# Kernel optimization log

Measured on AMD Instinct MI355X. Metric: run time of the kernel, lower is better.

## Reference

```python
import jax, jax.numpy as jnp
import numpy as np

N, M, D = 131072, 128, 128

def setup_inputs() -> dict:
    key = jax.random.key(0)
    k1, k2, k3 = jax.random.split(key, 3)
    X = jax.random.normal(k1, (N, D), dtype=jnp.float32)
    r = jax.random.uniform(k2, (N, M), dtype=jnp.float32)
    mus = jax.random.normal(k3, (M, D), dtype=jnp.float32)
    return {"X": X, "r": r, "mus": mus}

def reference(X, r, mus):
    # Squared pairwise L2 distances without materializing [N, M, D]:
    x2 = jnp.sum(X * X, axis=1)            # [N]
    mu2 = jnp.sum(mus * mus, axis=1)       # [M]
    cross = X @ mus.T                      # [N, M]
    dist2 = jnp.maximum(x2[:, None] + mu2[None, :] - 2.0 * cross, 0.0)
    loss = jnp.sum(r * dist2) / X.shape[0]
    return loss
```

## Files before the change

### kernel.cpp

```cpp
#include <hip/hip_runtime.h>
#include <hip/hip_bf16.h>


typedef __attribute__((ext_vector_type(8)))  short  short8;
typedef __attribute__((ext_vector_type(16))) float  float16v;

#if defined(__has_builtin)
#if __has_builtin(__builtin_amdgcn_cvt_pk_bf16_f32)
#define HAVE_PK_BF16 1
#endif
#endif

__device__ __forceinline__ unsigned int pk_bf16(float x, float y) {
#ifdef HAVE_PK_BF16
    typedef __attribute__((ext_vector_type(2))) __bf16 bf16x2;
    bf16x2 p = __builtin_amdgcn_cvt_pk_bf16_f32(x, y);
    return __builtin_bit_cast(unsigned int, p);
#else
    unsigned int ux = __float_as_uint(x);
    unsigned int uy = __float_as_uint(y);
    ux += 0x7fffu + ((ux >> 16) & 1u);
    uy += 0x7fffu + ((uy >> 16) & 1u);
    return (ux >> 16) | (uy & 0xffff0000u);
#endif
}

__global__ void zero_out_kernel(float* out) { out[0] = 0.0f; }

__global__ __launch_bounds__(256, 4)
void isoloss_kernel(const float* __restrict__ X,
                    const float* __restrict__ r,
                    const float* __restrict__ mus,
                    float* __restrict__ out)
{
    const int tid  = threadIdx.x;
    const int wave = tid >> 6;
    const int lane = tid & 63;
    const int col  = lane & 31;
    const int half = lane >> 5;

    __shared__ float wsum[4];

    short8 bfrag[8];
    float mu2p = 0.0f;
    {
        const float* mrow = mus + (size_t)(wave * 32 + col) * 128 + half * 8;
        #pragma unroll
        for (int ks = 0; ks < 8; ++ks) {
            const float4 a = *(const float4*)(mrow + ks * 16);
            const float4 b = *(const float4*)(mrow + ks * 16 + 4);
            mu2p += a.x*a.x + a.y*a.y + a.z*a.z + a.w*a.w
                  + b.x*b.x + b.y*b.y + b.z*b.z + b.w*b.w;
            union { short8 s8; uint4 u4; } u;
            u.u4.x = pk_bf16(a.x, a.y);
            u.u4.y = pk_bf16(a.z, a.w);
            u.u4.z = pk_bf16(b.x, b.y);
            u.u4.w = pk_bf16(b.z, b.w);
            bfrag[ks] = u.s8;
        }
    }
    const float mu2 = mu2p + __shfl_xor(mu2p, 32);

    float s = 0.0f;

    for (int g = blockIdx.x; g < 4096; g += gridDim.x) {
        const int rowbase = g * 32;
        const float* xp = X + (size_t)(rowbase + col) * 128 + half * 8;
        const float* rp = r + (size_t)rowbase * 128 + wave * 32 + col;

        float rv[16];
        #pragma unroll
        for (int reg = 0; reg < 16; ++reg) {
            const int rl = (reg & 3) + 8 * (reg >> 2) + 4 * half;
            rv[reg] = rp[(size_t)rl * 128];
        }

        float16v acc = {};
        float p = 0.0f;
        #pragma unroll
        for (int ks = 0; ks < 8; ++ks) {
            const float4 a = *(const float4*)(xp + ks * 16);
            const float4 b = *(const float4*)(xp + ks * 16 + 4);
            p += a.x*a.x + a.y*a.y + a.z*a.z + a.w*a.w
               + b.x*b.x + b.y*b.y + b.z*b.z + b.w*b.w;
            union { short8 s8; uint4 u4; } u;
            u.u4.x = pk_bf16(a.x, a.y);
            u.u4.y = pk_bf16(a.z, a.w);
            u.u4.z = pk_bf16(b.x, b.y);
            u.u4.w = pk_bf16(b.z, b.w);
            acc = __builtin_amdgcn_mfma_f32_32x32x16_bf16(u.s8, bfrag[ks], acc, 0, 0, 0);
        }
        const float x2v = p + __shfl_xor(p, 32);

        #pragma unroll
        for (int reg = 0; reg < 16; ++reg) {
            const int rl = (reg & 3) + 8 * (reg >> 2) + 4 * half;
            const float x2r = __shfl(x2v, rl);
            float d = fmaxf(x2r + mu2 - 2.0f * acc[reg], 0.0f);
            s += rv[reg] * d;
        }
    }

    #pragma unroll
    for (int off = 32; off > 0; off >>= 1) s += __shfl_down(s, off);
    if (lane == 0) wsum[wave] = s;
    __syncthreads();
    if (tid == 0) {
        const float t = wsum[0] + wsum[1] + wsum[2] + wsum[3];
        atomicAdd(out, t * (1.0f / 131072.0f));
    }
}

extern "C" void kernel_launch(void* const* d_in, const int* in_sizes, int n_in,
                              void* d_out, int out_size, void* d_ws, size_t ws_size,
                              hipStream_t stream) {
    const float* X   = (const float*)d_in[0];
    const float* r   = (const float*)d_in[1];
    const float* mus = (const float*)d_in[2];
    float* out = (float*)d_out;

    zero_out_kernel<<<1, 1, 0, stream>>>(out);
    isoloss_kernel<<<1024, 256, 0, stream>>>(X, r, mus, out);
}
```

Measured before the change: 171.8 us.

## Stage X tile in LDS as bf16 once per block and spread atomics

Each block now loads its 128-row X tile once with coalesced loads, computes row norms and bf16 conversions once, and stores them in LDS. All four waves then share them instead of each reloading and converting the same rows. The final sum goes through 64 workspace slots and a separate reduce kernel to reduce atomic contention. LDS use and register pressure increase, occupancy bounds drop, and there is an extra kernel launch.

```diff
diff --git a/kernel.cpp b/kernel.cpp
--- a/kernel.cpp
+++ b/kernel.cpp
@@ -4,6 +4,8 @@
 
 typedef __attribute__((ext_vector_type(8)))  short  short8;
 typedef __attribute__((ext_vector_type(16))) float  float16v;
+
+#define LDSP 136
 
 #if defined(__has_builtin)
 #if __has_builtin(__builtin_amdgcn_cvt_pk_bf16_f32)
@@ -25,21 +27,55 @@
 #endif
 }
 
-__global__ void zero_out_kernel(float* out) { out[0] = 0.0f; }
+__global__ void zero_ws_kernel(float* ws) { ws[threadIdx.x] = 0.0f; }
 
-__global__ __launch_bounds__(256, 4)
+__global__ void final_reduce_kernel(const float* ws, float* out) {
+    const int lane = threadIdx.x;
+    float t = ws[lane];
+    #pragma unroll
+    for (int off = 32; off > 0; off >>= 1) t += __shfl_down(t, off);
+    if (lane == 0) out[0] = t * (1.0f / 131072.0f);
+}
+
+__global__ __launch_bounds__(256, 3)
 void isoloss_kernel(const float* __restrict__ X,
                     const float* __restrict__ r,
                     const float* __restrict__ mus,
-                    float* __restrict__ out)
+                    float* __restrict__ ws)
 {
     const int tid  = threadIdx.x;
+    const int blk  = blockIdx.x;
     const int wave = tid >> 6;
     const int lane = tid & 63;
     const int col  = lane & 31;
     const int half = lane >> 5;
 
+    __shared__ unsigned short ldsA[128 * LDSP];
+    __shared__ float x2s[128];
     __shared__ float wsum[4];
+
+    const float* xbase = X + (size_t)blk * 128 * 128;
+    float4 xv[16];
+    #pragma unroll
+    for (int it = 0; it < 16; ++it)
+        xv[it] = *(const float4*)(xbase + (size_t)(it * 256 + tid) * 4);
+
+    #pragma unroll
+    for (int it = 0; it < 16; ++it) {
+        const float4 v = xv[it];
+        float p = v.x*v.x + v.y*v.y + v.z*v.z + v.w*v.w;
+        p += __shfl_xor(p, 16);
+        p += __shfl_xor(p, 8);
+        p += __shfl_xor(p, 4);
+        p += __shfl_xor(p, 2);
+        p += __shfl_xor(p, 1);
+        const int row = it * 8 + (tid >> 5);
+        if ((tid & 31) == 0) x2s[row] = p;
+        uint2 h;
+        h.x = pk_bf16(v.x, v.y);
+        h.y = pk_bf16(v.z, v.w);
+        *(uint2*)&ldsA[row * LDSP + (tid & 31) * 4] = h;
+    }
 
     short8 bfrag[8];
     float mu2p = 0.0f;
@@ -61,13 +97,12 @@
     }
     const float mu2 = mu2p + __shfl_xor(mu2p, 32);
 
+    __syncthreads();
+
     float s = 0.0f;
-
-    for (int g = blockIdx.x; g < 4096; g += gridDim.x) {
-        const int rowbase = g * 32;
-        const float* xp = X + (size_t)(rowbase + col) * 128 + half * 8;
-        const float* rp = r + (size_t)rowbase * 128 + wave * 32 + col;
-
+    #pragma unroll
+    for (int mt = 0; mt < 4; ++mt) {
+        const float* rp = r + (size_t)(blk * 128 + mt * 32) * 128 + wave * 32 + col;
         float rv[16];
         #pragma unroll
         for (int reg = 0; reg < 16; ++reg) {
@@ -76,27 +111,20 @@
         }
 
         float16v acc = {};
-        float p = 0.0f;
         #pragma unroll
         for (int ks = 0; ks < 8; ++ks) {
-            const float4 a = *(const float4*)(xp + ks * 16);
-            const float4 b = *(const float4*)(xp + ks * 16 + 4);
-            p += a.x*a.x + a.y*a.y + a.z*a.z + a.w*a.w
-               + b.x*b.x + b.y*b.y + b.z*b.z + b.w*b.w;
-            union { short8 s8; uint4 u4; } u;
-            u.u4.x = pk_bf16(a.x, a.y);
-            u.u4.y = pk_bf16(a.z, a.w);
-            u.u4.z = pk_bf16(b.x, b.y);
-            u.u4.w = pk_bf16(b.z, b.w);
-            acc = __builtin_amdgcn_mfma_f32_32x32x16_bf16(u.s8, bfrag[ks], acc, 0, 0, 0);
+            const short8 af = *(const short8*)&ldsA[(mt * 32 + col) * LDSP + ks * 16 + half * 8];
+            acc = __builtin_amdgcn_mfma_f32_32x32x16_bf16(af, bfrag[ks], acc, 0, 0, 0);
         }
-        const float x2v = p + __shfl_xor(p, 32);
+
+        float4 xq[4];
+        #pragma unroll
+        for (int q = 0; q < 4; ++q)
+            xq[q] = *(const float4*)&x2s[mt * 32 + q * 8 + half * 4];
 
         #pragma unroll
         for (int reg = 0; reg < 16; ++reg) {
-            const int rl = (reg & 3) + 8 * (reg >> 2) + 4 * half;
-            const float x2r = __shfl(x2v, rl);
-            float d = fmaxf(x2r + mu2 - 2.0f * acc[reg], 0.0f);
+            const float d = fmaxf(xq[reg >> 2][reg & 3] + mu2 - 2.0f * acc[reg], 0.0f);
             s += rv[reg] * d;
         }
     }
@@ -105,10 +133,8 @@
     for (int off = 32; off > 0; off >>= 1) s += __shfl_down(s, off);
     if (lane == 0) wsum[wave] = s;
     __syncthreads();
-    if (tid == 0) {
-        const float t = wsum[0] + wsum[1] + wsum[2] + wsum[3];
-        atomicAdd(out, t * (1.0f / 131072.0f));
-    }
+    if (tid == 0)
+        atomicAdd(&ws[blk & 63], wsum[0] + wsum[1] + wsum[2] + wsum[3]);
 }
 
 extern "C" void kernel_launch(void* const* d_in, const int* in_sizes, int n_in,
@@ -118,7 +144,9 @@
     const float* r   = (const float*)d_in[1];
     const float* mus = (const float*)d_in[2];
     float* out = (float*)d_out;
+    float* ws  = (float*)d_ws;
 
-    zero_out_kernel<<<1, 1, 0, stream>>>(out);
-    isoloss_kernel<<<1024, 256, 0, stream>>>(X, r, mus, out);
+    zero_ws_kernel<<<1, 64, 0, stream>>>(ws);
+    isoloss_kernel<<<1024, 256, 0, stream>>>(X, r, mus, ws);
+    final_reduce_kernel<<<1, 64, 0, stream>>>(ws, out);
 }
```

Measured after the change: 151.0 us. -12.1%, faster.

## Swap MFMA operands for vectorized r loads, prefetch X, spread atomics

Applied to the files above, without the earlier changes.

Swaps the MFMA A/B operands so each lane's accumulator holds a row of contiguous centroid columns, which lets r be read with float4 loads instead of 16 scalar strided loads. X is now loaded in two halves, with the second half issued as software prefetch inside the k-loop. mu2 values are pre-shuffled once outside the loop, which removes the per-element shuffles of x2. The single-address atomic is replaced by 64 workspace slots plus a final reduction kernel, at the cost of an extra launch. Launch bounds are lowered to 3 blocks per CU, giving more registers per thread.

```diff
diff --git a/kernel.cpp b/kernel.cpp
--- a/kernel.cpp
+++ b/kernel.cpp
@@ -25,13 +25,21 @@
 #endif
 }
 
-__global__ void zero_out_kernel(float* out) { out[0] = 0.0f; }
+__global__ void zero_ws_kernel(float* ws) { ws[threadIdx.x] = 0.0f; }
 
-__global__ __launch_bounds__(256, 4)
+__global__ void final_reduce_kernel(const float* ws, float* out) {
+    const int lane = threadIdx.x;
+    float t = ws[lane];
+    #pragma unroll
+    for (int off = 32; off > 0; off >>= 1) t += __shfl_down(t, off);
+    if (lane == 0) out[0] = t * (1.0f / 131072.0f);
+}
+
+__global__ __launch_bounds__(256, 3)
 void isoloss_kernel(const float* __restrict__ X,
                     const float* __restrict__ r,
                     const float* __restrict__ mus,
-                    float* __restrict__ out)
+                    float* __restrict__ ws)
 {
     const int tid  = threadIdx.x;
     const int wave = tid >> 6;
@@ -60,27 +68,43 @@
         }
     }
     const float mu2 = mu2p + __shfl_xor(mu2p, 32);
+    float4 mu2q[4];
+    #pragma unroll
+    for (int q = 0; q < 4; ++q) {
+        mu2q[q].x = __shfl(mu2, q * 8 + half * 4 + 0);
+        mu2q[q].y = __shfl(mu2, q * 8 + half * 4 + 1);
+        mu2q[q].z = __shfl(mu2, q * 8 + half * 4 + 2);
+        mu2q[q].w = __shfl(mu2, q * 8 + half * 4 + 3);
+    }
 
     float s = 0.0f;
 
     for (int g = blockIdx.x; g < 4096; g += gridDim.x) {
         const int rowbase = g * 32;
         const float* xp = X + (size_t)(rowbase + col) * 128 + half * 8;
-        const float* rp = r + (size_t)rowbase * 128 + wave * 32 + col;
+        const float* rp = r + (size_t)(rowbase + col) * 128 + wave * 32 + half * 4;
 
-        float rv[16];
+        float4 xa[4], xb[4];
         #pragma unroll
-        for (int reg = 0; reg < 16; ++reg) {
-            const int rl = (reg & 3) + 8 * (reg >> 2) + 4 * half;
-            rv[reg] = rp[(size_t)rl * 128];
+        for (int j = 0; j < 4; ++j) {
+            xa[j] = *(const float4*)(xp + j * 16);
+            xb[j] = *(const float4*)(xp + j * 16 + 4);
         }
+        float4 rv[4];
+        #pragma unroll
+        for (int q = 0; q < 4; ++q)
+            rv[q] = *(const float4*)(rp + q * 8);
 
         float16v acc = {};
         float p = 0.0f;
         #pragma unroll
         for (int ks = 0; ks < 8; ++ks) {
-            const float4 a = *(const float4*)(xp + ks * 16);
-            const float4 b = *(const float4*)(xp + ks * 16 + 4);
+            const float4 a = xa[ks & 3];
+            const float4 b = xb[ks & 3];
+            if (ks < 4) {
+                xa[ks & 3] = *(const float4*)(xp + (ks + 4) * 16);
+                xb[ks & 3] = *(const float4*)(xp + (ks + 4) * 16 + 4);
+            }
             p += a.x*a.x + a.y*a.y + a.z*a.z + a.w*a.w
                + b.x*b.x + b.y*b.y + b.z*b.z + b.w*b.w;
             union { short8 s8; uint4 u4; } u;
@@ -88,16 +112,18 @@
             u.u4.y = pk_bf16(a.z, a.w);
             u.u4.z = pk_bf16(b.x, b.y);
             u.u4.w = pk_bf16(b.z, b.w);
-            acc = __builtin_amdgcn_mfma_f32_32x32x16_bf16(u.s8, bfrag[ks], acc, 0, 0, 0);
+            acc = __builtin_amdgcn_mfma_f32_32x32x16_bf16(bfrag[ks], u.s8, acc, 0, 0, 0);
         }
         const float x2v = p + __shfl_xor(p, 32);
 
         #pragma unroll
-        for (int reg = 0; reg < 16; ++reg) {
-            const int rl = (reg & 3) + 8 * (reg >> 2) + 4 * half;
-            const float x2r = __shfl(x2v, rl);
-            float d = fmaxf(x2r + mu2 - 2.0f * acc[reg], 0.0f);
-            s += rv[reg] * d;
+        for (int q = 0; q < 4; ++q) {
+            const float4 rq = rv[q];
+            const float4 m2 = mu2q[q];
+            s += rq.x * fmaxf(x2v + m2.x - 2.0f * acc[q * 4 + 0], 0.0f);
+            s += rq.y * fmaxf(x2v + m2.y - 2.0f * acc[q * 4 + 1], 0.0f);
+            s += rq.z * fmaxf(x2v + m2.z - 2.0f * acc[q * 4 + 2], 0.0f);
+            s += rq.w * fmaxf(x2v + m2.w - 2.0f * acc[q * 4 + 3], 0.0f);
         }
     }
 
@@ -105,10 +131,8 @@
     for (int off = 32; off > 0; off >>= 1) s += __shfl_down(s, off);
     if (lane == 0) wsum[wave] = s;
     __syncthreads();
-    if (tid == 0) {
-        const float t = wsum[0] + wsum[1] + wsum[2] + wsum[3];
-        atomicAdd(out, t * (1.0f / 131072.0f));
-    }
+    if (tid == 0)
+        atomicAdd(&ws[blockIdx.x & 63], wsum[0] + wsum[1] + wsum[2] + wsum[3]);
 }
 
 extern "C" void kernel_launch(void* const* d_in, const int* in_sizes, int n_in,
@@ -118,7 +142,9 @@
     const float* r   = (const float*)d_in[1];
     const float* mus = (const float*)d_in[2];
     float* out = (float*)d_out;
+    float* ws  = (float*)d_ws;
 
-    zero_out_kernel<<<1, 1, 0, stream>>>(out);
-    isoloss_kernel<<<1024, 256, 0, stream>>>(X, r, mus, out);
+    zero_ws_kernel<<<1, 64, 0, stream>>>(ws);
+    isoloss_kernel<<<1024, 256, 0, stream>>>(X, r, mus, ws);
+    final_reduce_kernel<<<1, 64, 0, stream>>>(ws, out);
 }
```

New measurement: 165.1 us. 3.9% less time.
